# Optimization experiments

Hardware: AMD Instinct MI355X
Metric: run time of the kernel (lower is better)

Reference implementation:

```python
import jax, jax.numpy as jnp
import numpy as np
from jax import lax

HEADS = 8
AGENT = 49            # agent_num
POOL = 7              # int(sqrt(agent_num))
DOWN_H, DOWN_W = 7, 7  # downstream_agent_shape
DIM = 256
WIN = 56              # sqrt(num_patches)


def _resize(x, oh, ow):
    # torch F.interpolate(mode='bilinear', align_corners=False) equivalent for upsample/identity
    return jax.image.resize(x, x.shape[:-2] + (oh, ow), method='bilinear', antialias=False)


def _bias_pipeline(bias, H, W):
    # bias: (heads, AGENT, h0, w0) -> (heads, H*W, DOWN_H*DOWN_W)
    h = bias.shape[0]
    pb = _resize(bias, H, W)                                     # (h, 49, H, W)
    pb = pb.reshape(h, POOL, POOL, H * W).transpose(0, 3, 1, 2)  # (h, HW, 7, 7)
    pb = _resize(pb, DOWN_H, DOWN_W)                             # (h, HW, 7, 7)
    return pb.reshape(h, H * W, DOWN_H * DOWN_W)


def setup_inputs() -> dict:
    key = jax.random.key(0)
    ks = jax.random.split(key, 16)
    b, H, W = 16, WIN, WIN
    n, c, h = H * W, DIM, HEADS
    s = 0.02
    f32 = jnp.float32
    return {
        "x": jax.random.normal(ks[0], (b, n, c), f32),
        "H": H,
        "W": W,
        "Wq": jax.random.normal(ks[1], (c, c), f32) * c ** -0.5,
        "Wkv": jax.random.normal(ks[2], (2 * c, c), f32) * c ** -0.5,
        "Wproj": jax.random.normal(ks[3], (c, c), f32) * c ** -0.5,
        "bproj": jnp.zeros((c,), f32),
        "dwc_w": jax.random.normal(ks[4], (c, 1, 3, 3), f32) * 0.1,
        "dwc_b": jnp.zeros((c,), f32),
        "an_bias": jax.random.normal(ks[5], (h, AGENT, 7, 7), f32) * s,
        "na_bias": jax.random.normal(ks[6], (h, AGENT, 7, 7), f32) * s,
        "ah_bias": jax.random.normal(ks[7], (1, h, AGENT, WIN, 1), f32) * s,
        "aw_bias": jax.random.normal(ks[8], (1, h, AGENT, 1, WIN), f32) * s,
        "ha_bias": jax.random.normal(ks[9], (1, h, WIN, 1, AGENT), f32) * s,
        "wa_bias": jax.random.normal(ks[10], (1, h, 1, WIN, AGENT), f32) * s,
    }


def reference(x, H, W, Wq, Wkv, Wproj, bproj, dwc_w, dwc_b,
              an_bias, na_bias, ah_bias, aw_bias, ha_bias, wa_bias):
    b, n, c = x.shape
    h = HEADS
    hd = c // h
    T = n // 2
    scale = hd ** -0.5
    dan = DOWN_H * DOWN_W

    q_lin = x @ Wq.T                       # (b,n,c)
    kv = x @ Wkv.T                         # (b,n,2c)
    k_lin, v_lin = kv[..., :c], kv[..., c:]

    # adaptive avg pool of q to (7,7) agent grid (H, W divisible by 7)
    qg = q_lin.reshape(b, DOWN_H, H // DOWN_H, DOWN_W, W // DOWN_W, c).mean(axis=(2, 4))
    agent = qg.reshape(b, dan, h, hd).transpose(0, 2, 1, 3)   # (b,h,49,hd)

    q = q_lin.reshape(b, n, h, hd).transpose(0, 2, 1, 3)      # (b,h,n,hd)
    k = k_lin.reshape(b, n, h, hd).transpose(0, 2, 1, 3)
    v = v_lin.reshape(b, n, h, hd).transpose(0, 2, 1, 3)

    # agent -> kv attention biases
    pb1 = _bias_pipeline(an_bias, H, W).transpose(0, 2, 1)    # (h,49,HW)
    pb2 = _bias_pipeline((ah_bias + aw_bias)[0], H, W).transpose(0, 2, 1)
    position_bias = (pb1 + pb2)[None]                         # (1,h,49,HW)

    agent_attn = jax.nn.softmax(
        jnp.einsum('bhad,bhnd->bhan', agent * scale, k) + position_bias, axis=-1)
    agent_v = jnp.einsum('bhan,bhnd->bhad', agent_attn, v)    # (b,h,49,hd)

    # query -> agent attention biases
    ab1 = _bias_pipeline(na_bias, H, W)                       # (h,HW,49)
    ab2 = _bias_pipeline((ha_bias + wa_bias)[0].transpose(0, 3, 1, 2), H, W)
    agent_bias = (ab1 + ab2)[None]                            # (1,h,HW,49)

    # top-T query selection, then bilinear upsample of scores back to n rows
    token_w = jax.nn.softmax(q.mean(axis=-1), axis=-1)        # (b,h,n)
    _, top_idx = lax.top_k(token_w, T)                        # (b,h,T)
    q_top = jnp.take_along_axis(q, top_idx[..., None], axis=2)  # (b,h,T,hd)
    q2 = jnp.einsum('bhtd,bhad->bhta', q_top, agent)          # (b,h,T,49)
    q2 = _resize(q2, n, dan) * scale                          # (b,h,n,49)

    q_attn = jax.nn.softmax(q2 + agent_bias, axis=-1)
    out = jnp.einsum('bhna,bhad->bhnd', q_attn, agent_v)
    out = out.transpose(0, 2, 1, 3).reshape(b, n, c)

    # depthwise conv branch on v
    v_img = v.transpose(0, 2, 1, 3).reshape(b, H, W, c).transpose(0, 3, 1, 2)  # (b,c,H,W)
    dw = lax.conv_general_dilated(v_img, dwc_w, (1, 1), ((1, 1), (1, 1)),
                                  feature_group_count=c)
    dw = dw + dwc_b[None, :, None, None]
    out = out + dw.transpose(0, 2, 3, 1).reshape(b, n, c)
    return out @ Wproj.T + bproj
```

## Files before the change

kernel.cpp:

```cpp
#include <hip/hip_runtime.h>
#include <stdint.h>

typedef _Float16 f16;
typedef _Float16 half8 __attribute__((ext_vector_type(8)));
typedef float f32x4 __attribute__((ext_vector_type(4)));

#define NBATCH 16
#define NTOK 3136
#define NTOT 50176
#define NH 8
#define NA 49
#define NAP 64
#define TTOP 1568
#define SCALE 0.17677669529663687f
#define FPARTS 4

__device__ __forceinline__ f32x4 mfma16(half8 a, half8 b, f32x4 c) {
  return __builtin_amdgcn_mfma_f32_16x16x32_f16(a, b, c, 0, 0, 0);
}

__device__ __forceinline__ void gload16(const void* g, void* l) {
  __builtin_amdgcn_global_load_lds(
      (const __attribute__((address_space(1))) void*)g,
      (__attribute__((address_space(3))) void*)l, 16, 0, 0);
}

__global__ __launch_bounds__(256) void k_prep_w(const float* Wq, const float* Wkv, const float* Wproj,
                                                f16* wqkv, f16* wproj) {
  int total1 = 768 * 256;
  int total = total1 + 256 * 256;
  for (int i = blockIdx.x * 256 + threadIdx.x; i < total; i += gridDim.x * 256) {
    if (i < total1) {
      int j = i >> 8, k = i & 255;
      float v = (j < 256) ? Wq[j * 256 + k] : Wkv[(j - 256) * 256 + k];
      wqkv[i] = (f16)v;
    } else {
      int i2 = i - total1;
      wproj[i2] = (f16)Wproj[i2];
    }
  }
}

__global__ __launch_bounds__(256) void k_cvt_x(const float* x, f16* xh, long total) {
  long i = (long)blockIdx.x * blockDim.x + threadIdx.x;
  long stride = (long)gridDim.x * blockDim.x;
  for (long e = i * 8; e < total; e += stride * 8) {
    float4 v0 = *(const float4*)(x + e);
    float4 v1 = *(const float4*)(x + e + 4);
    half8 o = {(f16)v0.x, (f16)v0.y, (f16)v0.z, (f16)v0.w,
               (f16)v1.x, (f16)v1.y, (f16)v1.z, (f16)v1.w};
    *(half8*)(xh + e) = o;
  }
}

__global__ __launch_bounds__(256) void k_bias(const float* an_b, const float* na_b,
                                              const float* ah_b, const float* aw_b,
                                              const float* ha_b, const float* wa_b,
                                              float* pos_bias, float* agent_bias) {
  int n = blockIdx.x * 256 + threadIdx.x;
  int h = blockIdx.y;
  if (n >= NTOK) return;
  int y = n / 56, x = n - y * 56;
  float py = (y + 0.5f) * 0.125f - 0.5f;
  float px = (x + 0.5f) * 0.125f - 0.5f;
  int iy0 = (int)floorf(py); float fy = py - (float)iy0;
  int ix0 = (int)floorf(px); float fx = px - (float)ix0;
  int y0 = max(iy0, 0), y1 = min(iy0 + 1, 6);
  int x0 = max(ix0, 0), x1 = min(ix0 + 1, 6);
  float w00 = (1.f - fy) * (1.f - fx), w01 = (1.f - fy) * fx;
  float w10 = fy * (1.f - fx), w11 = fy * fx;
  for (int a = 0; a < NA; ++a) {
    const float* pa = an_b + (h * NA + a) * 49;
    float up_an = w00 * pa[y0 * 7 + x0] + w01 * pa[y0 * 7 + x1] +
                  w10 * pa[y1 * 7 + x0] + w11 * pa[y1 * 7 + x1];
    const float* pn = na_b + (h * NA + a) * 49;
    float up_na = w00 * pn[y0 * 7 + x0] + w01 * pn[y0 * 7 + x1] +
                  w10 * pn[y1 * 7 + x0] + w11 * pn[y1 * 7 + x1];
    float pb = up_an + ah_b[(h * NA + a) * 56 + y] + aw_b[(h * NA + a) * 56 + x];
    pos_bias[((size_t)(h * NAP + a)) * NTOK + n] = pb;
    float ab = up_na + ha_b[(h * 56 + y) * NA + a] + wa_b[(h * 56 + x) * NA + a];
    agent_bias[((size_t)(h * NAP + a)) * NTOK + n] = ab;
  }
  for (int a = NA; a < NAP; ++a)
    pos_bias[((size_t)(h * NAP + a)) * NTOK + n] = 0.f;
}

template <bool PROJ>
__global__ __launch_bounds__(256) void k_gemm(const f16* __restrict__ A, const f16* __restrict__ Bw,
                                              f16* __restrict__ CH, float* __restrict__ Cf32,
                                              const float* __restrict__ bias, int N) {
  __shared__ __align__(16) char lds[16384];
  int per = gridDim.x >> 3;
  int wrk = (blockIdx.x & 7) * per + (blockIdx.x >> 3);
  int nNT = N >> 7;
  int mt = wrk / nNT, nt = wrk - mt * nNT;
  int m0 = mt * 128, n0 = nt * 128;
  int tid = threadIdx.x, w = tid >> 6, l = tid & 63, lr = l & 15, lg = l >> 4;
  int wm = w >> 1, wn = w & 1;
  f32x4 acc[4][4] = {};
  const char* Bb = (const char*)Bw + (size_t)n0 * 512;
  int rowA0 = 32 * w + (l >> 2);
  int rowA1 = rowA0 + 16;
  int koff = (l & 3) * 16;
  char* ldsA0 = lds + (2 * w) * 1024;
  char* ldsA1 = lds + (2 * w + 1) * 1024;
  char* ldsB0 = lds + 8192 + (2 * w) * 1024;
  char* ldsB1 = lds + 8192 + (2 * w + 1) * 1024;

  for (int k0 = 0; k0 < 256; k0 += 32) {
    if (PROJ) {
      const char* Ab = (const char*)A + ((size_t)(k0 >> 5) * NTOT + m0) * 64;
      gload16(Ab + (size_t)rowA0 * 64 + koff, ldsA0);
      gload16(Ab + (size_t)rowA1 * 64 + koff, ldsA1);
    } else {
      const char* Ab = (const char*)A + (size_t)m0 * 512 + k0 * 2;
      gload16(Ab + (size_t)rowA0 * 512 + koff, ldsA0);
      gload16(Ab + (size_t)rowA1 * 512 + koff, ldsA1);
    }
    gload16(Bb + (size_t)rowA0 * 512 + k0 * 2 + koff, ldsB0);
    gload16(Bb + (size_t)rowA1 * 512 + k0 * 2 + koff, ldsB1);
    __syncthreads();
    half8 af[4], bf[4];
#pragma unroll
    for (int m4 = 0; m4 < 4; ++m4) {
      int row = wm * 64 + m4 * 16 + lr;
      af[m4] = *(const half8*)(lds + row * 64 + lg * 16);
    }
#pragma unroll
    for (int n4 = 0; n4 < 4; ++n4) {
      int row = wn * 64 + n4 * 16 + lr;
      bf[n4] = *(const half8*)(lds + 8192 + row * 64 + lg * 16);
    }
#pragma unroll
    for (int m4 = 0; m4 < 4; ++m4)
#pragma unroll
      for (int n4 = 0; n4 < 4; ++n4)
        acc[m4][n4] = mfma16(af[m4], bf[n4], acc[m4][n4]);
    __syncthreads();
  }

  if (PROJ) {
#pragma unroll
    for (int n4 = 0; n4 < 4; ++n4) {
      int n = n0 + wn * 64 + n4 * 16 + lr;
#pragma unroll
      for (int m4 = 0; m4 < 4; ++m4)
#pragma unroll
        for (int r = 0; r < 4; ++r) {
          int m = m0 + wm * 64 + m4 * 16 + lg * 4 + r;
          Cf32[(size_t)m * N + n] = acc[m4][n4][r] + bias[n];
        }
    }
  } else {
    f16* cl = (f16*)lds;
    int rr = tid >> 2, c4 = tid & 3;
#pragma unroll
    for (int hm = 0; hm < 2; ++hm) {
      __syncthreads();
      if (wm == hm) {
#pragma unroll
        for (int m4 = 0; m4 < 4; ++m4)
#pragma unroll
          for (int n4 = 0; n4 < 4; ++n4)
#pragma unroll
            for (int r = 0; r < 4; ++r)
              cl[(m4 * 16 + lg * 4 + r) * 128 + wn * 64 + n4 * 16 + lr] = (f16)acc[m4][n4][r];
      }
      __syncthreads();
#pragma unroll
      for (int cc = 0; cc < 4; ++cc) {
        int pn = (n0 >> 5) + cc;
        half8 v = *(const half8*)(cl + rr * 128 + cc * 32 + c4 * 8);
        *(half8*)(CH + ((size_t)pn * NTOT + m0 + hm * 64 + rr) * 32 + c4 * 8) = v;
      }
    }
  }
}

__global__ __launch_bounds__(256) void k_pool_tw(const f16* qkvH, f16* agent, float* tw) {
  int bh = blockIdx.x, b = bh >> 3, h = bh & 7;
  int tid = threadIdx.x;
  const f16* qp0 = qkvH + ((size_t)h * NTOT + (size_t)b * NTOK) * 32;
  {
    int a = tid >> 2, c = tid & 3;
    float s8[8] = {};
    if (a < NA) {
      int dh = a / 7, dwi = a - dh * 7;
      for (int i = 0; i < 8; ++i)
#pragma unroll
        for (int j = 0; j < 8; ++j) {
          int tok = (dh * 8 + i) * 56 + dwi * 8 + j;
          half8 v = *(const half8*)(qp0 + (size_t)tok * 32 + c * 8);
#pragma unroll
          for (int e = 0; e < 8; ++e) s8[e] += (float)v[e];
        }
    }
    half8 o;
#pragma unroll
    for (int e = 0; e < 8; ++e) o[e] = (f16)(s8[e] * (SCALE / 64.f));
    *(half8*)(agent + (size_t)bh * NAP * 32 + a * 32 + c * 8) = o;
  }
  for (int n = tid; n < NTOK; n += 256) {
    const half8* qp = (const half8*)(qp0 + (size_t)n * 32);
    float sum = 0.f;
#pragma unroll
    for (int j = 0; j < 4; ++j) {
      half8 v = qp[j];
#pragma unroll
      for (int e = 0; e < 8; ++e) sum += (float)v[e];
    }
    tw[(size_t)bh * NTOK + n] = sum * (1.f / 32.f);
  }
}

template <int NE, int J>
__device__ __forceinline__ void stage_local(unsigned long long (&key)[NE], int kmask, int base) {
#pragma unroll
  for (int e = 0; e < NE; ++e) {
    if ((e & J) == 0) {
      bool desc = (((base + e) & kmask) == 0);
      unsigned long long a = key[e], c = key[e | J];
      if ((a < c) == desc) { key[e] = c; key[e | J] = a; }
    }
  }
}

__global__ __launch_bounds__(256, 1) void k_sort1(const float* tw, unsigned long long* keys64) {
  __shared__ unsigned long long lk[2048 + 128];
  int bh = blockIdx.x >> 1, half = blockIdx.x & 1;
  int tid = threadIdx.x;
  const float* p = tw + (size_t)bh * NTOK;
  int gbase = half * 2048 + tid * 8;
  unsigned long long key[8];
#pragma unroll
  for (int e = 0; e < 8; ++e) {
    int s = gbase + e;
    float v = (s < NTOK) ? p[s] : -1e30f;
    unsigned ub = __float_as_uint(v);
    ub = (ub & 0x80000000u) ? ~ub : (ub | 0x80000000u);
    unsigned low = (s < NTOK) ? ~(unsigned)s : 0u;
    key[e] = ((unsigned long long)ub << 32) | low;
  }
  stage_local<8, 1>(key, 2, gbase);
  stage_local<8, 2>(key, 4, gbase); stage_local<8, 1>(key, 4, gbase);
  stage_local<8, 4>(key, 8, gbase); stage_local<8, 2>(key, 8, gbase); stage_local<8, 1>(key, 8, gbase);
  for (int k = 16; k <= 2048; k <<= 1) {
    bool desc = ((gbase & k) == 0);
    for (int j = k >> 1; j >= 8; j >>= 1) {
      int m = j >> 3;
      bool takeMax = (((tid & m) == 0) == desc);
      unsigned long long pv[8];
      if (m <= 32) {
#pragma unroll
        for (int e = 0; e < 8; ++e) pv[e] = __shfl_xor(key[e], m, 64);
      } else {
        __syncthreads();
#pragma unroll
        for (int e = 0; e < 8; ++e) { int ix = tid * 8 + e; lk[ix + (ix >> 4)] = key[e]; }
        __syncthreads();
        int pb = (tid ^ m) * 8;
#pragma unroll
        for (int e = 0; e < 8; ++e) { int ix = pb + e; pv[e] = lk[ix + (ix >> 4)]; }
      }
#pragma unroll
      for (int e = 0; e < 8; ++e)
        key[e] = takeMax ? (key[e] > pv[e] ? key[e] : pv[e])
                         : (key[e] < pv[e] ? key[e] : pv[e]);
    }
    stage_local<8, 4>(key, k, gbase);
    stage_local<8, 2>(key, k, gbase);
    stage_local<8, 1>(key, k, gbase);
  }
  unsigned long long* op = keys64 + (size_t)bh * 4096 + gbase;
#pragma unroll
  for (int e = 0; e < 8; ++e) op[e] = key[e];
}

__global__ __launch_bounds__(256, 1) void k_sort2(const unsigned long long* keys64, int* topidx) {
  __shared__ unsigned long long lk[4096 + 256];
  int bh = blockIdx.x, tid = threadIdx.x;
  const unsigned long long* ip = keys64 + (size_t)bh * 4096 + (size_t)tid * 16;
  unsigned long long key[16];
#pragma unroll
  for (int e = 0; e < 16; ++e) key[e] = ip[e];
  int base = tid * 16;
  for (int j = 2048; j >= 16; j >>= 1) {
    int m = j >> 4;
    bool takeMax = ((tid & m) == 0);
    unsigned long long pv[16];
    if (m <= 32) {
#pragma unroll
      for (int e = 0; e < 16; ++e) pv[e] = __shfl_xor(key[e], m, 64);
    } else {
      __syncthreads();
#pragma unroll
      for (int e = 0; e < 16; ++e) { int ix = base + e; lk[ix + (ix >> 4)] = key[e]; }
      __syncthreads();
      int pb = (tid ^ m) * 16;
#pragma unroll
      for (int e = 0; e < 16; ++e) { int ix = pb + e; pv[e] = lk[ix + (ix >> 4)]; }
    }
#pragma unroll
    for (int e = 0; e < 16; ++e)
      key[e] = takeMax ? (key[e] > pv[e] ? key[e] : pv[e])
                       : (key[e] < pv[e] ? key[e] : pv[e]);
  }
  stage_local<16, 8>(key, 4096, base);
  stage_local<16, 4>(key, 4096, base);
  stage_local<16, 2>(key, 4096, base);
  stage_local<16, 1>(key, 4096, base);
  if (tid < TTOP / 16) {
    int* op = topidx + (size_t)bh * TTOP + base;
#pragma unroll
    for (int e = 0; e < 16; ++e) op[e] = (int)(~(unsigned)key[e]);
  }
}

__global__ __launch_bounds__(256) void k_vt(const f16* qkvH, f16* vt) {
  __shared__ __align__(16) f16 t[64][40];
  int bh = blockIdx.y, b = bh >> 3, h = bh & 7;
  int n0 = blockIdx.x * 64;
  int tid = threadIdx.x;
  const f16* vp = qkvH + ((size_t)(16 + h) * NTOT + (size_t)b * NTOK + n0) * 32;
  {
    int nl = tid >> 2, c = tid & 3;
    *(half8*)(&t[nl][c * 8]) = *(const half8*)(vp + (size_t)nl * 32 + c * 8);
  }
  __syncthreads();
  for (int s = tid; s < 64 * 32; s += 256) {
    int d = s >> 6, nl = s & 63;
    vt[((size_t)(bh * 32 + d)) * NTOK + n0 + nl] = t[nl][d];
  }
}

__global__ __launch_bounds__(256) void k_flash(const f16* qkvH, const f16* agent, const f16* vt,
                                               const float* pos_bias, float* opart, float* rspart) {
  __shared__ __align__(16) f16 pbuf[4][64][40];
  __shared__ float ored[64][33];
  __shared__ float rssum[64];
  int part = blockIdx.x, bh = blockIdx.y, b = bh >> 3, h = bh & 7;
  int tid = threadIdx.x, w = tid >> 6, l = tid & 63, lr = l & 15, lg = l >> 4;
  half8 afrag[4];
#pragma unroll
  for (int mt = 0; mt < 4; ++mt)
    afrag[mt] = *(const half8*)(agent + ((size_t)bh * 64 + mt * 16 + lr) * 32 + lg * 8);
  f32x4 o[4][2] = {};
  float rs[4][4] = {};
  const f16* kbase = qkvH + ((size_t)(8 + h) * NTOT + (size_t)b * NTOK) * 32;
  const f16* vtb = vt + (size_t)bh * 32 * NTOK;
  const float* pbb = pos_bias + (size_t)h * NAP * NTOK;
  f32x4 zero = {};
  for (int n0 = (part * 4 + w) * 32; n0 < NTOK; n0 += 512) {
#pragma unroll
    for (int t2 = 0; t2 < 2; ++t2) {
      int nc = n0 + t2 * 16;
      half8 kf = *(const half8*)(kbase + (size_t)(nc + lr) * 32 + lg * 8);
#pragma unroll
      for (int mt = 0; mt < 4; ++mt) {
        f32x4 s = mfma16(afrag[mt], kf, zero);
#pragma unroll
        for (int r = 0; r < 4; ++r) {
          int a = mt * 16 + lg * 4 + r;
          float pv = __expf(s[r] + pbb[(size_t)a * NTOK + nc + lr]);
          rs[mt][r] += pv;
          pbuf[w][a][t2 * 16 + lr] = (f16)pv;
        }
      }
    }
    half8 pf[4];
#pragma unroll
    for (int mt = 0; mt < 4; ++mt)
      pf[mt] = *(const half8*)(&pbuf[w][mt * 16 + lr][lg * 8]);
#pragma unroll
    for (int dt = 0; dt < 2; ++dt) {
      half8 vf = *(const half8*)(vtb + (size_t)(dt * 16 + lr) * NTOK + n0 + lg * 8);
#pragma unroll
      for (int mt = 0; mt < 4; ++mt)
        o[mt][dt] = mfma16(pf[mt], vf, o[mt][dt]);
    }
  }
#pragma unroll
  for (int mt = 0; mt < 4; ++mt)
#pragma unroll
    for (int r = 0; r < 4; ++r) {
      float v = rs[mt][r];
      for (int off = 1; off < 16; off <<= 1) v += __shfl_xor(v, off, 64);
      rs[mt][r] = v;
    }
  for (int s = tid; s < 64 * 33; s += 256) ((float*)ored)[s] = 0.f;
  if (tid < 64) rssum[tid] = 0.f;
  __syncthreads();
  for (int ww = 0; ww < 4; ++ww) {
    if (w == ww) {
      if (lr == 0)
#pragma unroll
        for (int mt = 0; mt < 4; ++mt)
#pragma unroll
          for (int r = 0; r < 4; ++r) rssum[mt * 16 + lg * 4 + r] += rs[mt][r];
#pragma unroll
      for (int mt = 0; mt < 4; ++mt)
#pragma unroll
        for (int dt = 0; dt < 2; ++dt)
#pragma unroll
          for (int r = 0; r < 4; ++r)
            ored[mt * 16 + lg * 4 + r][dt * 16 + lr] += o[mt][dt][r];
    }
    __syncthreads();
  }
  int pp = bh * FPARTS + part;
  for (int s = tid; s < NA * 32; s += 256) {
    int a = s >> 5, d = s & 31;
    opart[((size_t)pp * 64 + a) * 32 + d] = ored[a][d];
  }
  if (tid < NA) rspart[(size_t)pp * 64 + tid] = rssum[tid];
}

__global__ __launch_bounds__(256) void k_fred(const float* opart, const float* rspart, float* agv) {
  int bh = blockIdx.x, tid = threadIdx.x;
  for (int s = tid; s < NA * 32; s += 256) {
    int a = s >> 5, d = s & 31;
    float o = 0.f, rs = 0.f;
#pragma unroll
    for (int p = 0; p < FPARTS; ++p) {
      int pp = bh * FPARTS + p;
      o += opart[((size_t)pp * 64 + a) * 32 + d];
      rs += rspart[(size_t)pp * 64 + a];
    }
    agv[(size_t)bh * NA * 32 + s] = o / rs;
  }
}

__global__ __launch_bounds__(256) void k_po(const f16* __restrict__ qkvH, const f16* __restrict__ agent,
                                            const int* __restrict__ topidx,
                                            const float* __restrict__ agent_bias,
                                            const float* __restrict__ agent_v,
                                            const float* __restrict__ dwc_w,
                                            const float* __restrict__ dwc_b,
                                            f16* __restrict__ preH) {
  __shared__ __align__(16) char uq[18432];
  __shared__ __align__(16) f16 pbuf[14 * 8 * 16 * 8];
  __shared__ __align__(16) f16 avT[32][72];
  __shared__ float wconv[9][32];
  __shared__ float bconv[32];
  f16 (*q2buf)[72] = (f16(*)[72])uq;
  f16 (*ctile)[40] = (f16(*)[40])uq;
  int chunk = blockIdx.x, bh = blockIdx.y, b = bh >> 3, h = bh & 7;
  int tid = threadIdx.x, w = tid >> 6, l = tid & 63, lr = l & 15, lg = l >> 4;
  const f16* qplane = qkvH + ((size_t)h * NTOT + (size_t)b * NTOK) * 32;
  const f16* vp = qkvH + ((size_t)(16 + h) * NTOT + (size_t)b * NTOK) * 32;
  for (int s = tid; s < 32 * 64; s += 256) {
    int d = s >> 6, a = s & 63;
    avT[d][a] = (a < NA) ? (f16)agent_v[((size_t)bh * NA + a) * 32 + d] : (f16)0.f;
  }
  for (int s = tid; s < 32 * 9; s += 256) {
    int d = s / 9, t = s - d * 9;
    wconv[t][d] = dwc_w[(size_t)(h * 32 + d) * 9 + t];
  }
  if (tid < 32) bconv[tid] = dwc_b[h * 32 + tid];
  half8 bfrag[4];
#pragma unroll
  for (int nt = 0; nt < 4; ++nt)
    bfrag[nt] = *(const half8*)(agent + ((size_t)bh * 64 + nt * 16 + lr) * 32 + lg * 8);
  int jbase = chunk * 112 - 8;
  f32x4 zero = {};
  for (int mt = w; mt < 8; mt += 4) {
    int j = jbase + mt * 16 + lr;
    int jc = min(max(j, 0), TTOP - 1);
    int tok = topidx[(size_t)bh * TTOP + jc];
    half8 qf = *(const half8*)(qplane + (size_t)tok * 32 + lg * 8);
#pragma unroll
    for (int nt = 0; nt < 4; ++nt) {
      f32x4 s = mfma16(qf, bfrag[nt], zero);
#pragma unroll
      for (int r = 0; r < 4; ++r)
        q2buf[mt * 16 + lg * 4 + r][nt * 16 + lr] = (f16)s[r];
    }
  }
  __syncthreads();
  if (tid < 224) {
    int g = chunk * 224 + tid;
    int hi = g >> 1;
    int jA, jB; float wAq, wBq;
    if (g & 1) { jA = hi; jB = hi + 1; wAq = 0.75f; wBq = 0.25f; }
    else       { jA = hi - 1; jB = hi; wAq = 0.25f; wBq = 0.75f; }
    jA = min(max(jA, 0), TTOP - 1);
    jB = min(max(jB, 0), TTOP - 1);
    int lA = jA - jbase, lB = jB - jbase;
    const float* ab = agent_bias + (size_t)h * NAP * NTOK + g;
    float ssum = 0.f;
    half8 oo[7];
#pragma unroll
    for (int c = 0; c < 7; ++c) {
      half8 a8 = *(const half8*)(&q2buf[lA][c * 8]);
      half8 b8 = *(const half8*)(&q2buf[lB][c * 8]);
#pragma unroll
      for (int e = 0; e < 8; ++e) {
        int a = c * 8 + e;
        float pv = 0.f;
        if (a < NA) {
          float v = wAq * (float)a8[e] + wBq * (float)b8[e] + ab[(size_t)a * NTOK];
          pv = __expf(v);
          ssum += pv;
        }
        oo[c][e] = (f16)pv;
      }
    }
    f16 invs = (f16)(1.f / ssum);
    half8 iv8 = {invs, invs, invs, invs, invs, invs, invs, invs};
    int lt = tid >> 4, lrr = tid & 15;
#pragma unroll
    for (int c = 0; c < 7; ++c)
      *(half8*)(pbuf + ((size_t)(lt * 8 + c) * 16 + lrr) * 8) = oo[c] * iv8;
    half8 z = {};
    *(half8*)(pbuf + ((size_t)(lt * 8 + 7) * 16 + lrr) * 8) = z;
  }
  __syncthreads();
  half8 bf[2][2];
#pragma unroll
  for (int nt = 0; nt < 2; ++nt)
#pragma unroll
    for (int ks = 0; ks < 2; ++ks)
      bf[nt][ks] = *(const half8*)(&avT[0][0] + (size_t)(nt * 16 + lr) * 72 + ks * 32 + lg * 8);
#pragma unroll
  for (int i = 0; i < 4; ++i) {
    int lt = w * 4 + i;
    if (lt >= 14) continue;
    half8 pa0 = *(const half8*)(pbuf + ((size_t)(lt * 8 + lg) * 16 + lr) * 8);
    half8 pa1 = *(const half8*)(pbuf + ((size_t)(lt * 8 + 4 + lg) * 16 + lr) * 8);
    f32x4 acc0 = {}, acc1 = {};
    acc0 = mfma16(pa0, bf[0][0], acc0);
    acc0 = mfma16(pa1, bf[0][1], acc0);
    acc1 = mfma16(pa0, bf[1][0], acc1);
    acc1 = mfma16(pa1, bf[1][1], acc1);
    int ltrow = lt * 16 + lg * 4;
#pragma unroll
    for (int r = 0; r < 4; ++r) {
      ctile[ltrow + r][lr] = (f16)acc0[r];
      ctile[ltrow + r][16 + lr] = (f16)acc1[r];
    }
  }
  __syncthreads();
  if (tid >= 224) return;
  int g = chunk * 224 + tid;
  int y0 = chunk * 4;
  int ly = tid / 56, x = tid - ly * 56;
  int y = y0 + ly;
  float accd[32];
#pragma unroll
  for (int c = 0; c < 4; ++c) {
    half8 cv = *(const half8*)(&ctile[tid][c * 8]);
#pragma unroll
    for (int e = 0; e < 8; ++e) accd[c * 8 + e] = (float)cv[e] + bconv[c * 8 + e];
  }
#pragma unroll
  for (int ky = 0; ky < 3; ++ky) {
    int gy = y + ky - 1;
    if (gy < 0 || gy >= 56) continue;
#pragma unroll
    for (int kx = 0; kx < 3; ++kx) {
      int xx = x + kx - 1;
      if (xx < 0 || xx >= 56) continue;
      int t = ky * 3 + kx;
      const f16* vt9 = vp + (size_t)(gy * 56 + xx) * 32;
#pragma unroll
      for (int c = 0; c < 4; ++c) {
        half8 vv = *(const half8*)(vt9 + c * 8);
#pragma unroll
        for (int e = 0; e < 8; ++e) accd[c * 8 + e] += wconv[t][c * 8 + e] * (float)vv[e];
      }
    }
  }
  f16* op = preH + ((size_t)h * NTOT + (size_t)b * NTOK + g) * 32;
#pragma unroll
  for (int c = 0; c < 4; ++c) {
    half8 o;
#pragma unroll
    for (int e = 0; e < 8; ++e) o[e] = (f16)accd[c * 8 + e];
    *(half8*)(op + c * 8) = o;
  }
}

extern "C" void kernel_launch(void* const* d_in, const int* in_sizes, int n_in,
                              void* d_out, int out_size, void* d_ws, size_t ws_size,
                              hipStream_t stream) {
  const float* x     = (const float*)d_in[0];
  const float* Wq    = (const float*)d_in[3];
  const float* Wkv   = (const float*)d_in[4];
  const float* Wproj = (const float*)d_in[5];
  const float* bproj = (const float*)d_in[6];
  const float* dwc_w = (const float*)d_in[7];
  const float* dwc_b = (const float*)d_in[8];
  const float* an_b  = (const float*)d_in[9];
  const float* na_b  = (const float*)d_in[10];
  const float* ah_b  = (const float*)d_in[11];
  const float* aw_b  = (const float*)d_in[12];
  const float* ha_b  = (const float*)d_in[13];
  const float* wa_b  = (const float*)d_in[14];

  char* ws = (char*)d_ws;
  size_t off = 0;
  auto alloc = [&](size_t bytes) {
    void* p = ws + off;
    off = (off + bytes + 255) & ~(size_t)255;
    return p;
  };
  f16* wqkv    = (f16*)alloc((size_t)768 * 256 * 2);
  f16* wproj   = (f16*)alloc((size_t)256 * 256 * 2);
  f16* qkvH    = (f16*)alloc((size_t)24 * NTOT * 32 * 2);
  float* posb  = (float*)alloc((size_t)8 * NAP * NTOK * 4);
  float* agb   = (float*)alloc((size_t)8 * NAP * NTOK * 4);
  f16* agent   = (f16*)alloc((size_t)128 * NAP * 32 * 2);
  float* tw    = (float*)alloc((size_t)128 * NTOK * 4);
  int* topidx  = (int*)alloc((size_t)128 * TTOP * 4);
  unsigned long long* keys64 = (unsigned long long*)alloc((size_t)128 * 4096 * 8);
  f16* vt      = (f16*)alloc((size_t)128 * 32 * NTOK * 2);
  float* agv   = (float*)alloc((size_t)128 * NA * 32 * 4);
  float* opart = (float*)alloc((size_t)128 * FPARTS * 64 * 32 * 4);
  float* rspart= (float*)alloc((size_t)128 * FPARTS * 64 * 4);
  f16* preH    = (f16*)alloc((size_t)8 * NTOT * 32 * 2);
  f16* xh      = (f16*)alloc((size_t)NTOT * 256 * 2);

  k_prep_w<<<1024, 256, 0, stream>>>(Wq, Wkv, Wproj, wqkv, wproj);
  k_cvt_x<<<2048, 256, 0, stream>>>(x, xh, (long)NTOT * 256);
  k_bias<<<dim3(13, 8), 256, 0, stream>>>(an_b, na_b, ah_b, aw_b, ha_b, wa_b, posb, agb);
  k_gemm<false><<<2352, 256, 0, stream>>>(xh, wqkv, qkvH, nullptr, nullptr, 768);
  k_pool_tw<<<128, 256, 0, stream>>>(qkvH, agent, tw);
  k_sort1<<<256, 256, 0, stream>>>(tw, keys64);
  k_sort2<<<128, 256, 0, stream>>>(keys64, topidx);
  k_vt<<<dim3(49, 128), 256, 0, stream>>>(qkvH, vt);
  k_flash<<<dim3(FPARTS, 128), 256, 0, stream>>>(qkvH, agent, vt, posb, opart, rspart);
  k_fred<<<128, 256, 0, stream>>>(opart, rspart, agv);
  k_po<<<dim3(14, 128), 256, 0, stream>>>(qkvH, agent, topidx, agb, agv, dwc_w, dwc_b, preH);
  k_gemm<true><<<784, 256, 0, stream>>>(preH, wproj, nullptr, (float*)d_out, bproj, 256);
}
```

Before: 225.5 us.

## Halve k_po chunk size and split channels across two threads per token

k_po now handles 112 tokens per block instead of 224, launching twice as many blocks. Each token's softmax and conv work is split across two threads, each owning half the agent columns or channels, with the softmax sum combined through a lane shuffle. The aim is more parallelism, shorter per-thread serial work and less shared memory per block for better occupancy. The cost is redundant per-block setup (avT, conv weights, agent fragments) repeated across twice as many blocks.

```diff
diff --git a/kernel.cpp b/kernel.cpp
--- a/kernel.cpp
+++ b/kernel.cpp
@@ -437,8 +437,8 @@
                                             const float* __restrict__ dwc_w,
                                             const float* __restrict__ dwc_b,
                                             f16* __restrict__ preH) {
-  __shared__ __align__(16) char uq[18432];
-  __shared__ __align__(16) f16 pbuf[14 * 8 * 16 * 8];
+  __shared__ __align__(16) char uq[9216];
+  __shared__ __align__(16) f16 pbuf[7 * 8 * 16 * 8];
   __shared__ __align__(16) f16 avT[32][72];
   __shared__ float wconv[9][32];
   __shared__ float bconv[32];
@@ -461,10 +461,10 @@
 #pragma unroll
   for (int nt = 0; nt < 4; ++nt)
     bfrag[nt] = *(const half8*)(agent + ((size_t)bh * 64 + nt * 16 + lr) * 32 + lg * 8);
-  int jbase = chunk * 112 - 8;
+  int jbase = chunk * 56 - 4;
   f32x4 zero = {};
-  for (int mt = w; mt < 8; mt += 4) {
-    int j = jbase + mt * 16 + lr;
+  {
+    int j = jbase + w * 16 + lr;
     int jc = min(max(j, 0), TTOP - 1);
     int tok = topidx[(size_t)bh * TTOP + jc];
     half8 qf = *(const half8*)(qplane + (size_t)tok * 32 + lg * 8);
@@ -473,12 +473,13 @@
       f32x4 s = mfma16(qf, bfrag[nt], zero);
 #pragma unroll
       for (int r = 0; r < 4; ++r)
-        q2buf[mt * 16 + lg * 4 + r][nt * 16 + lr] = (f16)s[r];
+        q2buf[w * 16 + lg * 4 + r][nt * 16 + lr] = (f16)s[r];
     }
   }
   __syncthreads();
   if (tid < 224) {
-    int g = chunk * 224 + tid;
+    int ltok = tid >> 1, hc = tid & 1;
+    int g = chunk * 112 + ltok;
     int hi = g >> 1;
     int jA, jB; float wAq, wBq;
     if (g & 1) { jA = hi; jB = hi + 1; wAq = 0.75f; wBq = 0.25f; }
@@ -488,9 +489,10 @@
     int lA = jA - jbase, lB = jB - jbase;
     const float* ab = agent_bias + (size_t)h * NAP * NTOK + g;
     float ssum = 0.f;
-    half8 oo[7];
-#pragma unroll
-    for (int c = 0; c < 7; ++c) {
+    half8 oo[4];
+#pragma unroll
+    for (int cc = 0; cc < 4; ++cc) {
+      int c = hc * 4 + cc;
       half8 a8 = *(const half8*)(&q2buf[lA][c * 8]);
       half8 b8 = *(const half8*)(&q2buf[lB][c * 8]);
 #pragma unroll
@@ -502,17 +504,18 @@
           pv = __expf(v);
           ssum += pv;
         }
-        oo[c][e] = (f16)pv;
+        oo[cc][e] = (f16)pv;
       }
     }
+    ssum += __shfl_xor(ssum, 1, 64);
     f16 invs = (f16)(1.f / ssum);
     half8 iv8 = {invs, invs, invs, invs, invs, invs, invs, invs};
-    int lt = tid >> 4, lrr = tid & 15;
-#pragma unroll
-    for (int c = 0; c < 7; ++c)
-      *(half8*)(pbuf + ((size_t)(lt * 8 + c) * 16 + lrr) * 8) = oo[c] * iv8;
-    half8 z = {};
-    *(half8*)(pbuf + ((size_t)(lt * 8 + 7) * 16 + lrr) * 8) = z;
+    int lt = ltok >> 4, lrr = ltok & 15;
+#pragma unroll
+    for (int cc = 0; cc < 4; ++cc) {
+      int c = hc * 4 + cc;
+      *(half8*)(pbuf + ((size_t)(lt * 8 + c) * 16 + lrr) * 8) = oo[cc] * iv8;
+    }
   }
   __syncthreads();
   half8 bf[2][2];
@@ -522,9 +525,9 @@
     for (int ks = 0; ks < 2; ++ks)
       bf[nt][ks] = *(const half8*)(&avT[0][0] + (size_t)(nt * 16 + lr) * 72 + ks * 32 + lg * 8);
 #pragma unroll
-  for (int i = 0; i < 4; ++i) {
-    int lt = w * 4 + i;
-    if (lt >= 14) continue;
+  for (int i = 0; i < 2; ++i) {
+    int lt = w * 2 + i;
+    if (lt >= 7) continue;
     half8 pa0 = *(const half8*)(pbuf + ((size_t)(lt * 8 + lg) * 16 + lr) * 8);
     half8 pa1 = *(const half8*)(pbuf + ((size_t)(lt * 8 + 4 + lg) * 16 + lr) * 8);
     f32x4 acc0 = {}, acc1 = {};
@@ -541,16 +544,16 @@
   }
   __syncthreads();
   if (tid >= 224) return;
-  int g = chunk * 224 + tid;
-  int y0 = chunk * 4;
-  int ly = tid / 56, x = tid - ly * 56;
-  int y = y0 + ly;
-  float accd[32];
-#pragma unroll
-  for (int c = 0; c < 4; ++c) {
-    half8 cv = *(const half8*)(&ctile[tid][c * 8]);
-#pragma unroll
-    for (int e = 0; e < 8; ++e) accd[c * 8 + e] = (float)cv[e] + bconv[c * 8 + e];
+  int ltok = tid >> 1, hc = tid & 1;
+  int g = chunk * 112 + ltok;
+  int ly = ltok / 56, x = ltok - ly * 56;
+  int y = chunk * 2 + ly;
+  float accd[16];
+#pragma unroll
+  for (int c = 0; c < 2; ++c) {
+    half8 cv = *(const half8*)(&ctile[ltok][hc * 16 + c * 8]);
+#pragma unroll
+    for (int e = 0; e < 8; ++e) accd[c * 8 + e] = (float)cv[e] + bconv[hc * 16 + c * 8 + e];
   }
 #pragma unroll
   for (int ky = 0; ky < 3; ++ky) {
@@ -561,18 +564,18 @@
       int xx = x + kx - 1;
       if (xx < 0 || xx >= 56) continue;
       int t = ky * 3 + kx;
-      const f16* vt9 = vp + (size_t)(gy * 56 + xx) * 32;
-#pragma unroll
-      for (int c = 0; c < 4; ++c) {
+      const f16* vt9 = vp + (size_t)(gy * 56 + xx) * 32 + hc * 16;
+#pragma unroll
+      for (int c = 0; c < 2; ++c) {
         half8 vv = *(const half8*)(vt9 + c * 8);
 #pragma unroll
-        for (int e = 0; e < 8; ++e) accd[c * 8 + e] += wconv[t][c * 8 + e] * (float)vv[e];
+        for (int e = 0; e < 8; ++e) accd[c * 8 + e] += wconv[t][hc * 16 + c * 8 + e] * (float)vv[e];
       }
     }
   }
-  f16* op = preH + ((size_t)h * NTOT + (size_t)b * NTOK + g) * 32;
-#pragma unroll
-  for (int c = 0; c < 4; ++c) {
+  f16* op = preH + ((size_t)h * NTOT + (size_t)b * NTOK + g) * 32 + hc * 16;
+#pragma unroll
+  for (int c = 0; c < 2; ++c) {
     half8 o;
 #pragma unroll
     for (int e = 0; e < 8; ++e) o[e] = (f16)accd[c * 8 + e];
@@ -630,6 +633,6 @@
   k_vt<<<dim3(49, 128), 256, 0, stream>>>(qkvH, vt);
   k_flash<<<dim3(FPARTS, 128), 256, 0, stream>>>(qkvH, agent, vt, posb, opart, rspart);
   k_fred<<<128, 256, 0, stream>>>(opart, rspart, agv);
-  k_po<<<dim3(14, 128), 256, 0, stream>>>(qkvH, agent, topidx, agb, agv, dwc_w, dwc_b, preH);
+  k_po<<<dim3(28, 128), 256, 0, stream>>>(qkvH, agent, topidx, agb, agv, dwc_w, dwc_b, preH);
   k_gemm<true><<<784, 256, 0, stream>>>(preH, wproj, nullptr, (float*)d_out, bproj, 256);
 }
```

New measurement: 231.8 us (median of 2 runs). +2.8%, slower.
